# Optimization experiments

Hardware: AMD Instinct MI355X
Metric: run time of the kernel (lower is better)

The kernel has to match this reference:

```python
import jax, jax.numpy as jnp
import numpy as np

B, S, D, H, SPAN = 4, 1024, 768, 12, 512
HD = D // H  # 64


def setup_inputs() -> dict:
    key = jax.random.key(0)
    ks = jax.random.split(key, 8)
    hidden_states = jax.random.normal(ks[0], (B, S, D), jnp.float32)
    rel_embeddings = jax.random.normal(ks[1], (2 * SPAN, D), jnp.float32) * 0.02
    Wq = jax.random.normal(ks[2], (D, D), jnp.float32) * 0.02
    Wk = jax.random.normal(ks[3], (D, D), jnp.float32) * 0.02
    Wv = jax.random.normal(ks[4], (D, D), jnp.float32) * 0.02
    Wo = jax.random.normal(ks[5], (D, D), jnp.float32) * 0.02
    bq = jnp.zeros((D,), jnp.float32); bk = jnp.zeros((D,), jnp.float32)
    bv = jnp.zeros((D,), jnp.float32); bo = jnp.zeros((D,), jnp.float32)
    ln_g = jnp.ones((D,), jnp.float32); ln_b = jnp.zeros((D,), jnp.float32)
    idx = jnp.arange(S)
    relative_pos = (idx[:, None] - idx[None, :]).astype(jnp.int32)  # q - k
    lengths = jnp.array([1024, 896, 768, 512])  # padding-style mask
    valid = idx[None, :] < lengths[:, None]  # [B,S]
    attention_mask = (valid[:, :, None] & valid[:, None, :])[:, None, :, :].astype(jnp.int32)  # [B,1,S,S]
    return dict(hidden_states=hidden_states, rel_embeddings=rel_embeddings,
                Wq=Wq, bq=bq, Wk=Wk, bk=bk, Wv=Wv, bv=bv, Wo=Wo, bo=bo,
                ln_g=ln_g, ln_b=ln_b, attention_mask=attention_mask,
                relative_pos=relative_pos)


def reference(hidden_states, rel_embeddings, Wq, bq, Wk, bk, Wv, bv, Wo, bo,
              ln_g, ln_b, attention_mask, relative_pos):
    # content projections -> [B,H,S,HD]
    q = (hidden_states @ Wq.T + bq).reshape(B, S, H, HD).transpose(0, 2, 1, 3)
    k = (hidden_states @ Wk.T + bk).reshape(B, S, H, HD).transpose(0, 2, 1, 3)
    v = (hidden_states @ Wv.T + bv).reshape(B, S, H, HD).transpose(0, 2, 1, 3)

    scale_qk = jnp.sqrt(jnp.float32(HD * 3))  # scale_factor = 3
    scores = jnp.einsum('bhqd,bhkd->bhqk', q, k) / scale_qk

    # shared-key position projections -> [H, 2*SPAN, HD]
    pos_q = (rel_embeddings @ Wq.T + bq).reshape(2 * SPAN, H, HD).transpose(1, 0, 2)
    pos_k = (rel_embeddings @ Wk.T + bk).reshape(2 * SPAN, H, HD).transpose(1, 0, 2)

    rp = relative_pos.astype(jnp.int32)
    # c2p: query vs relative key-position embedding, gathered by clamp(rel+span)
    c2p_att = jnp.einsum('bhqd,hkd->bhqk', q, pos_k)  # [B,H,S,2*SPAN]
    c2p_pos = jnp.clip(rp + SPAN, 0, 2 * SPAN - 1)
    c2p_idx = jnp.broadcast_to(c2p_pos[None, None], (B, H, S, S))
    c2p = jnp.take_along_axis(c2p_att, c2p_idx, axis=-1) / scale_qk

    # p2c: key vs relative query-position embedding, gathered by clamp(-rel+span), then transposed
    p2c_att = jnp.einsum('bhkd,hqd->bhkq', k, pos_q)  # [B,H,S,2*SPAN]
    p2c_pos = jnp.clip(SPAN - rp, 0, 2 * SPAN - 1)
    p2c_idx = jnp.broadcast_to(p2c_pos[None, None], (B, H, S, S))
    p2c = jnp.swapaxes(jnp.take_along_axis(p2c_att, p2c_idx, axis=-1), -1, -2)
    p2c = p2c / jnp.sqrt(jnp.float32(HD))  # note: torch uses sqrt(d) here, no scale_factor

    scores = scores + c2p + p2c

    # XSoftmax: masked softmax with zeros at masked positions
    mask = attention_mask.astype(bool)  # [B,1,S,S]
    neg = jnp.finfo(scores.dtype).min
    probs = jax.nn.softmax(jnp.where(mask, scores, neg), axis=-1)
    probs = jnp.where(mask, probs, jnp.float32(0))

    ctx = jnp.einsum('bhqk,bhkd->bhqd', probs, v).transpose(0, 2, 1, 3).reshape(B, S, D)

    # DebertaV2SelfOutput: dense + residual + LayerNorm(eps=1e-7)
    x = ctx @ Wo.T + bo + hidden_states
    mu = x.mean(-1, keepdims=True)
    var = ((x - mu) ** 2).mean(-1, keepdims=True)
    return (x - mu) / jnp.sqrt(var + 1e-7) * ln_g + ln_b
```

## Files before the change

### kernel.cpp

```cpp
#include <hip/hip_runtime.h>
#include <hip/hip_bf16.h>
#include <stdint.h>

typedef __hip_bfloat16 bf16;
typedef __attribute__((ext_vector_type(8))) short s8v;
typedef __attribute__((ext_vector_type(4))) float f4v;

__device__ __align__(16) bf16 g_hidden[4096 * 768];
__device__ __align__(16) bf16 g_rel[1024 * 768];
__device__ __align__(16) bf16 g_Wqkv[2304 * 768];
__device__ __align__(16) bf16 g_Wo[768 * 768];
__device__ __align__(16) bf16 g_biasQKV[2304];
__device__ __align__(16) bf16 g_biasPos[1536];
__device__ __align__(16) bf16 g_bo[768];
__device__ __align__(16) bf16 g_lng[768];
__device__ __align__(16) bf16 g_lnb[768];
__device__ __align__(16) bf16 g_Y1[4096 * 1536];
__device__ __align__(16) bf16 g_VT[48u * 64 * 1024];
__device__ __align__(16) bf16 g_Yp[1024 * 1536];
__device__ __align__(16) bf16 g_ctx[4096 * 768];
__device__ __align__(16) float g_X[4096 * 768];
__device__ int g_vq[4096], g_vk[4096], g_kmax[4];

__device__ __forceinline__ float bfs(short x) {
  return __uint_as_float(((unsigned int)(unsigned short)x) << 16);
}
__device__ __forceinline__ unsigned short f2bf(float f) {
  bf16 h = __float2bfloat16(f);
  return *(unsigned short*)&h;
}
__device__ __forceinline__ bool detect_bf16(const void* lng_raw) {
  return *(const unsigned int*)lng_raw == 0x3F803F80u;
}

__device__ __forceinline__ void cvt4(const void* src, bf16* dst, long grp, bool isbf) {
  long e = grp * 4;
  if (isbf) {
    *(uint2*)(dst + e) = *(const uint2*)((const bf16*)src + e);
  } else {
    float4 f = *(const float4*)((const float*)src + e);
    union { unsigned short us[4]; uint2 v; } u;
    u.us[0] = f2bf(f.x); u.us[1] = f2bf(f.y); u.us[2] = f2bf(f.z); u.us[3] = f2bf(f.w);
    *(uint2*)(dst + e) = u.v;
  }
}

__global__ __launch_bounds__(256) void cvt_inputs(
    const void* h, const void* r,
    const void* wq, const void* wk, const void* wv, const void* wo,
    const void* bq, const void* bk, const void* bv, const void* bo,
    const void* lg, const void* lb)
{
  if (blockIdx.x == 0 && threadIdx.x < 4) g_kmax[threadIdx.x] = 0;
  const bool isbf = detect_bf16(lg);
  long i = (long)blockIdx.x * 256 + threadIdx.x;
  if (i < 786432) { cvt4(h,  g_hidden,          i, isbf); return; } i -= 786432;
  if (i < 196608) { cvt4(r,  g_rel,             i, isbf); return; } i -= 196608;
  if (i < 147456) { cvt4(wq, g_Wqkv,            i, isbf); return; } i -= 147456;
  if (i < 147456) { cvt4(wk, g_Wqkv + 589824,   i, isbf); return; } i -= 147456;
  if (i < 147456) { cvt4(wv, g_Wqkv + 1179648,  i, isbf); return; } i -= 147456;
  if (i < 147456) { cvt4(wo, g_Wo,              i, isbf); return; } i -= 147456;
  if (i < 192)    { cvt4(bq, g_biasQKV,         i, isbf); return; } i -= 192;
  if (i < 192)    { cvt4(bk, g_biasQKV + 768,   i, isbf); return; } i -= 192;
  if (i < 192)    { cvt4(bv, g_biasQKV + 1536,  i, isbf); return; } i -= 192;
  if (i < 192)    { cvt4(bq, g_biasPos,         i, isbf); return; } i -= 192;
  if (i < 192)    { cvt4(bk, g_biasPos + 768,   i, isbf); return; } i -= 192;
  if (i < 192)    { cvt4(lg, g_lng,             i, isbf); return; } i -= 192;
  if (i < 192)    { cvt4(lb, g_lnb,             i, isbf); return; }
}

__global__ __launch_bounds__(256) void mask_prep(const int* __restrict__ mask) {
  int t = blockIdx.x * 256 + threadIdx.x;
  int b = t >> 10, i = t & 1023;
  int vq = mask[((size_t)(b * 1024 + i)) * 1024];
  int vk = mask[((size_t)(b * 1024)) * 1024 + i];
  g_vq[t] = vq;
  g_vk[t] = vk;
  if (vq | vk) atomicMax(&g_kmax[b], i + 1);
}

__global__ __launch_bounds__(256, 2) void gemm_bt(int which) {
  __shared__ short As[128][72];
  __shared__ short Bs[128][72];

  const bf16 *A, *B; const bf16* bias;
  int lda, ldb, K, mode;
  const int m0 = blockIdx.y * 128, n0 = blockIdx.x * 128;

  if (which == 0) {
    A = g_hidden; lda = 768; B = g_Wqkv; ldb = 768; bias = g_biasQKV; K = 768;
    mode = (n0 >= 1536) ? 5 : 0;
  } else if (which == 1) {
    A = g_rel; lda = 768; B = g_Wqkv; ldb = 768; bias = g_biasPos; K = 768; mode = 1;
  } else {
    A = g_ctx; lda = 768; B = g_Wo; ldb = 768; bias = g_bo; K = 768; mode = 4;
  }

  const int tid = threadIdx.x, wave = tid >> 6, lane = tid & 63;
  const int quad = lane >> 4, l15 = lane & 15;
  const int wm = (wave >> 1) * 64, wn = (wave & 1) * 64;
  const int sr = tid >> 2, sc8 = (tid & 3) * 16;

  f4v acc[4][4];
#pragma unroll
  for (int i = 0; i < 4; i++)
#pragma unroll
    for (int j = 0; j < 4; j++) acc[i][j] = (f4v){0.f, 0.f, 0.f, 0.f};

  uint4 pa0, pa1, pa2, pa3, pb0, pb1, pb2, pb3;
#define LOAD_T(k0)                                                           \
  {                                                                          \
    const bf16* ap = A + (size_t)(m0 + sr) * lda + (k0) + sc8;               \
    const bf16* ap2 = A + (size_t)(m0 + sr + 64) * lda + (k0) + sc8;         \
    const bf16* bp = B + (size_t)(n0 + sr) * ldb + (k0) + sc8;               \
    const bf16* bp2 = B + (size_t)(n0 + sr + 64) * ldb + (k0) + sc8;         \
    pa0 = *(const uint4*)ap;  pa1 = *(const uint4*)(ap + 8);                 \
    pa2 = *(const uint4*)ap2; pa3 = *(const uint4*)(ap2 + 8);                \
    pb0 = *(const uint4*)bp;  pb1 = *(const uint4*)(bp + 8);                 \
    pb2 = *(const uint4*)bp2; pb3 = *(const uint4*)(bp2 + 8);                \
  }

  LOAD_T(0)
  for (int k0 = 0; k0 < K; k0 += 64) {
    __syncthreads();
    *(uint4*)&As[sr][sc8] = pa0;      *(uint4*)&As[sr][sc8 + 8] = pa1;
    *(uint4*)&As[sr + 64][sc8] = pa2; *(uint4*)&As[sr + 64][sc8 + 8] = pa3;
    *(uint4*)&Bs[sr][sc8] = pb0;      *(uint4*)&Bs[sr][sc8 + 8] = pb1;
    *(uint4*)&Bs[sr + 64][sc8] = pb2; *(uint4*)&Bs[sr + 64][sc8 + 8] = pb3;
    if (k0 + 64 < K) LOAD_T(k0 + 64)
    __syncthreads();

    s8v af[4][2], bfr[4][2];
#pragma unroll
    for (int mt = 0; mt < 4; mt++) {
      af[mt][0] = *(const s8v*)&As[wm + mt * 16 + l15][quad * 8];
      af[mt][1] = *(const s8v*)&As[wm + mt * 16 + l15][32 + quad * 8];
    }
#pragma unroll
    for (int nt = 0; nt < 4; nt++) {
      bfr[nt][0] = *(const s8v*)&Bs[wn + nt * 16 + l15][quad * 8];
      bfr[nt][1] = *(const s8v*)&Bs[wn + nt * 16 + l15][32 + quad * 8];
    }
#pragma unroll
    for (int mt = 0; mt < 4; mt++)
#pragma unroll
      for (int nt = 0; nt < 4; nt++) {
        acc[mt][nt] = __builtin_amdgcn_mfma_f32_16x16x32_bf16(af[mt][0], bfr[nt][0], acc[mt][nt], 0, 0, 0);
        acc[mt][nt] = __builtin_amdgcn_mfma_f32_16x16x32_bf16(af[mt][1], bfr[nt][1], acc[mt][nt], 0, 0, 0);
      }
  }
#undef LOAD_T

  float biasv[4];
#pragma unroll
  for (int nt = 0; nt < 4; nt++)
    biasv[nt] = bfs(*(const short*)&bias[n0 + wn + nt * 16 + l15]);

#pragma unroll
  for (int mt = 0; mt < 4; mt++) {
#pragma unroll
    for (int nt = 0; nt < 4; nt++) {
      const int mbase = m0 + wm + mt * 16 + quad * 4;
      const int n = n0 + wn + nt * 16 + l15;
      if (mode == 5) {
        const int dd = n - 1536, hv = dd >> 6, hd = dd & 63;
        const int bb = mbase >> 10, ss = mbase & 1023;
        float t0 = acc[mt][nt][0] + biasv[nt], t1 = acc[mt][nt][1] + biasv[nt];
        float t2 = acc[mt][nt][2] + biasv[nt], t3 = acc[mt][nt][3] + biasv[nt];
        uint2 pk;
        pk.x = (unsigned int)f2bf(t0) | ((unsigned int)f2bf(t1) << 16);
        pk.y = (unsigned int)f2bf(t2) | ((unsigned int)f2bf(t3) << 16);
        *(uint2*)(g_VT + (((size_t)(bb * 12 + hv) * 64 + hd) << 10) + ss) = pk;
        continue;
      }
#pragma unroll
      for (int reg = 0; reg < 4; reg++) {
        const int m = mbase + reg;
        float v = acc[mt][nt][reg] + biasv[nt];
        if (mode == 0) {
          g_Y1[(size_t)m * 1536 + n] = __float2bfloat16(v);
        } else if (mode == 1) {
          g_Yp[(size_t)m * 1536 + n] = __float2bfloat16(v);
        } else {
          v += bfs(*(const short*)&g_hidden[(size_t)m * 768 + n]);
          g_X[(size_t)m * 768 + n] = v;
        }
      }
    }
  }
}

__global__ __launch_bounds__(256, 2) void attn_mfma() {
  const int bh = blockIdx.y, b = bh / 12, hh = bh - b * 12;
  const int q0 = blockIdx.x * 64;
  const int tid = threadIdx.x, wave = tid >> 6, lane = tid & 63;
  const int quad = lane >> 4, l15 = lane & 15;
  const int kmax = g_kmax[b];

  if (q0 >= kmax) {
    uint4 zz = {0u, 0u, 0u, 0u};
#pragma unroll
    for (int s = tid; s < 512; s += 256) {
      int r = s >> 3, cc = (s & 7) * 8;
      *(uint4*)(g_ctx + (size_t)(b * 1024 + q0 + r) * 768 + hh * 64 + cc) = zz;
    }
    return;
  }

  __shared__ short Ks[64][72], VTs[64][72];
  __shared__ short BandA[128][72];
  __shared__ short BandB[128][72];
  __shared__ short Pl[4][16][72];
  short* C2Pl = &BandA[0][0];
  short* P2Cl = &BandB[0][0];

  const size_t qrow = (size_t)(b * 1024 + q0 + wave * 16 + l15) * 1536 + hh * 64;
  const s8v qf0 = *(const s8v*)(g_Y1 + qrow + quad * 8);
  const s8v qf1 = *(const s8v*)(g_Y1 + qrow + 32 + quad * 8);

  int vqr[4];
#pragma unroll
  for (int reg = 0; reg < 4; reg++)
    vqr[reg] = g_vq[b * 1024 + q0 + wave * 16 + quad * 4 + reg];

  f4v accO[4];
#pragma unroll
  for (int dt = 0; dt < 4; dt++) accO[dt] = (f4v){0.f, 0.f, 0.f, 0.f};
  float psum[4] = {0.f, 0.f, 0.f, 0.f};

  const int sr = tid >> 2, sc8 = (tid & 3) * 16;
  const int brow = tid >> 1, bcol = (tid & 1) * 32;
  const bf16* Kbase = g_Y1 + (size_t)(b * 1024) * 1536 + 768 + hh * 64;
  const bf16* Vbase = g_VT + ((size_t)bh << 16);
  const bf16* PKbase = g_Yp + 768 + hh * 64;
  const bf16* PQbase = g_Yp + hh * 64;

  uint4 rk0, rk1, rv0, rv1, rpk[4], rpq[4];
#define LOAD_A(k0)                                                         \
  {                                                                        \
    const bf16* kp = Kbase + (size_t)((k0) + sr) * 1536 + sc8;             \
    rk0 = *(const uint4*)kp; rk1 = *(const uint4*)(kp + 8);                \
    const bf16* vp = Vbase + ((size_t)sr << 10) + (k0) + sc8;              \
    rv0 = *(const uint4*)vp; rv1 = *(const uint4*)(vp + 8);                \
    int jk = min(max(q0 - (k0) + 449 + brow, 0), 1023);                    \
    const bf16* pk = PKbase + (size_t)jk * 1536 + bcol;                    \
    rpk[0] = *(const uint4*)pk;       rpk[1] = *(const uint4*)(pk + 8);    \
    rpk[2] = *(const uint4*)(pk + 16); rpk[3] = *(const uint4*)(pk + 24);  \
    int jq = min(max((k0) - q0 + 449 + brow, 0), 1023);                    \
    const bf16* pq = PQbase + (size_t)jq * 1536 + bcol;                    \
    rpq[0] = *(const uint4*)pq;       rpq[1] = *(const uint4*)(pq + 8);    \
    rpq[2] = *(const uint4*)(pq + 16); rpq[3] = *(const uint4*)(pq + 24);  \
  }

  LOAD_A(0)
  const float r192 = 0.0721687836487032f;
  const float r64 = 0.125f;

  for (int k0 = 0; k0 < kmax; k0 += 64) {
    __syncthreads();
    *(uint4*)&Ks[sr][sc8] = rk0;   *(uint4*)&Ks[sr][sc8 + 8] = rk1;
    *(uint4*)&VTs[sr][sc8] = rv0;  *(uint4*)&VTs[sr][sc8 + 8] = rv1;
    *(uint4*)&BandA[brow][bcol] = rpk[0];      *(uint4*)&BandA[brow][bcol + 8] = rpk[1];
    *(uint4*)&BandA[brow][bcol + 16] = rpk[2]; *(uint4*)&BandA[brow][bcol + 24] = rpk[3];
    *(uint4*)&BandB[brow][bcol] = rpq[0];      *(uint4*)&BandB[brow][bcol + 8] = rpq[1];
    *(uint4*)&BandB[brow][bcol + 16] = rpq[2]; *(uint4*)&BandB[brow][bcol + 24] = rpq[3];
    if (k0 + 64 < kmax) LOAD_A(k0 + 64)
    __syncthreads();

    const s8v ka0 = *(const s8v*)&Ks[wave * 16 + l15][quad * 8];
    const s8v ka1 = *(const s8v*)&Ks[wave * 16 + l15][32 + quad * 8];

    f4v cacc[8], pacc[8];
#pragma unroll
    for (int nt2 = 0; nt2 < 8; nt2++) {
      s8v b0 = *(const s8v*)&BandA[nt2 * 16 + l15][quad * 8];
      s8v b1 = *(const s8v*)&BandA[nt2 * 16 + l15][32 + quad * 8];
      cacc[nt2] = __builtin_amdgcn_mfma_f32_16x16x32_bf16(qf0, b0, (f4v){0.f, 0.f, 0.f, 0.f}, 0, 0, 0);
      cacc[nt2] = __builtin_amdgcn_mfma_f32_16x16x32_bf16(qf1, b1, cacc[nt2], 0, 0, 0);
      s8v c0 = *(const s8v*)&BandB[nt2 * 16 + l15][quad * 8];
      s8v c1 = *(const s8v*)&BandB[nt2 * 16 + l15][32 + quad * 8];
      pacc[nt2] = __builtin_amdgcn_mfma_f32_16x16x32_bf16(ka0, c0, (f4v){0.f, 0.f, 0.f, 0.f}, 0, 0, 0);
      pacc[nt2] = __builtin_amdgcn_mfma_f32_16x16x32_bf16(ka1, c1, pacc[nt2], 0, 0, 0);
    }

    f4v sacc[4];
#pragma unroll
    for (int nt = 0; nt < 4; nt++) {
      s8v kb0 = *(const s8v*)&Ks[nt * 16 + l15][quad * 8];
      s8v kb1 = *(const s8v*)&Ks[nt * 16 + l15][32 + quad * 8];
      sacc[nt] = __builtin_amdgcn_mfma_f32_16x16x32_bf16(qf0, kb0, (f4v){0.f, 0.f, 0.f, 0.f}, 0, 0, 0);
      sacc[nt] = __builtin_amdgcn_mfma_f32_16x16x32_bf16(qf1, kb1, sacc[nt], 0, 0, 0);
    }

    __syncthreads();
#pragma unroll
    for (int nt2 = 0; nt2 < 8; nt2++) {
      const int col = nt2 * 16 + l15;
#pragma unroll
      for (int reg = 0; reg < 4; reg++) {
        const int row = wave * 16 + quad * 4 + reg;
        C2Pl[row * 130 + col] = (short)f2bf(cacc[nt2][reg]);
        P2Cl[row * 130 + col] = (short)f2bf(pacc[nt2][reg]);
      }
    }
    __syncthreads();

    const bool tail = (k0 + 64 > kmax);
#pragma unroll
    for (int nt = 0; nt < 4; nt++) {
      const int kl = nt * 16 + l15;
#pragma unroll
      for (int reg = 0; reg < 4; reg++) {
        const int ql = wave * 16 + quad * 4 + reg;
        float c2 = bfs(C2Pl[ql * 130 + (ql - kl + 63)]);
        float p2 = bfs(P2Cl[kl * 130 + (kl - ql + 63)]);
        float sc = (sacc[nt][reg] + c2) * r192 + p2 * r64;
        float pe = __expf(fminf(sc, 60.f));
        if (tail && (k0 + kl >= kmax)) pe = 0.f;
        psum[reg] += pe;
        Pl[wave][quad * 4 + reg][kl] = (short)f2bf(pe);
      }
    }

    s8v pa0 = *(const s8v*)&Pl[wave][l15][quad * 8];
    s8v pa1 = *(const s8v*)&Pl[wave][l15][32 + quad * 8];
#pragma unroll
    for (int dt = 0; dt < 4; dt++) {
      s8v vb0 = *(const s8v*)&VTs[dt * 16 + l15][quad * 8];
      s8v vb1 = *(const s8v*)&VTs[dt * 16 + l15][32 + quad * 8];
      accO[dt] = __builtin_amdgcn_mfma_f32_16x16x32_bf16(pa0, vb0, accO[dt], 0, 0, 0);
      accO[dt] = __builtin_amdgcn_mfma_f32_16x16x32_bf16(pa1, vb1, accO[dt], 0, 0, 0);
    }
  }
#undef LOAD_A

#pragma unroll
  for (int off = 1; off < 16; off <<= 1)
#pragma unroll
    for (int reg = 0; reg < 4; reg++) psum[reg] += __shfl_xor(psum[reg], off);

  float inv[4];
#pragma unroll
  for (int reg = 0; reg < 4; reg++)
    inv[reg] = (vqr[reg] != 0 && psum[reg] > 0.f) ? 1.f / psum[reg] : 0.f;

#pragma unroll
  for (int dt = 0; dt < 4; dt++)
#pragma unroll
    for (int reg = 0; reg < 4; reg++) {
      float v = accO[dt][reg] * inv[reg];
      g_ctx[(size_t)(b * 1024 + q0 + wave * 16 + quad * 4 + reg) * 768 + hh * 64 + dt * 16 + l15] =
          __float2bfloat16(v);
    }
}

__global__ __launch_bounds__(256) void ln_kernel(const void* lng_raw, void* out) {
  const bool isbf = detect_bf16(lng_raw);
  const int row = blockIdx.x;
  const int tid = threadIdx.x;
  const float* xr = g_X + (size_t)row * 768;
  float x0 = xr[tid], x1 = xr[tid + 256], x2 = xr[tid + 512];
  float s = x0 + x1 + x2;
  float s2 = x0 * x0 + x1 * x1 + x2 * x2;
#pragma unroll
  for (int off = 32; off; off >>= 1) { s += __shfl_xor(s, off); s2 += __shfl_xor(s2, off); }
  __shared__ float red[2][4];
  int w = tid >> 6, ln = tid & 63;
  if (ln == 0) { red[0][w] = s; red[1][w] = s2; }
  __syncthreads();
  float ts = red[0][0] + red[0][1] + red[0][2] + red[0][3];
  float ts2 = red[1][0] + red[1][1] + red[1][2] + red[1][3];
  float mu = ts * (1.f / 768.f);
  float var = fmaxf(ts2 * (1.f / 768.f) - mu * mu, 0.f);
  float rstd = rsqrtf(var + 1e-7f);
#pragma unroll
  for (int q = 0; q < 3; q++) {
    int cidx = tid + q * 256;
    float xv = (q == 0) ? x0 : (q == 1 ? x1 : x2);
    float gg = bfs(*(const short*)&g_lng[cidx]);
    float bb = bfs(*(const short*)&g_lnb[cidx]);
    float val = (xv - mu) * rstd * gg + bb;
    if (isbf) ((bf16*)out)[(size_t)row * 768 + cidx] = __float2bfloat16(val);
    else      ((float*)out)[(size_t)row * 768 + cidx] = val;
  }
}

extern "C" void kernel_launch(void* const* d_in, const int* in_sizes, int n_in,
                              void* d_out, int out_size, void* d_ws, size_t ws_size,
                              hipStream_t stream) {
  const int* amask = (const int*)d_in[12];
  (void)d_ws; (void)ws_size; (void)in_sizes; (void)n_in; (void)out_size;

  cvt_inputs<<<dim3(6150), 256, 0, stream>>>(
      d_in[0], d_in[1], d_in[2], d_in[4], d_in[6], d_in[8],
      d_in[3], d_in[5], d_in[7], d_in[9], d_in[10], d_in[11]);
  mask_prep<<<dim3(16), 256, 0, stream>>>(amask);
  gemm_bt<<<dim3(18, 32, 1), 256, 0, stream>>>(0);
  gemm_bt<<<dim3(12, 8, 1), 256, 0, stream>>>(1);
  attn_mfma<<<dim3(16, 48), 256, 0, stream>>>();
  gemm_bt<<<dim3(6, 32, 1), 256, 0, stream>>>(4);
  ln_kernel<<<dim3(4096), 256, 0, stream>>>(d_in[10], d_out);
}
```

Before: 395.2 us.

## Precompute c2p/p2c position scores in a separate band GEMM, gather in attention

Adds a band_gemm kernel that computes the full query×position and key×position score matrices for each (batch, head) into global bf16 buffers, skipping tiles outside the valid band. The attention kernel then gathers c2p and p2c values directly from these buffers. This replaces the in-loop band MFMAs, the LDS staging and the extra barriers, and also lowers LDS usage so the launch bound can allow more blocks per CU. The cost is a large intermediate (about 200 MB written and then read with scattered per-element gathers), which adds global memory traffic.

New measurement: 379.2 us. 4.0% less time.

```diff
diff --git a/kernel.cpp b/kernel.cpp
--- a/kernel.cpp
+++ b/kernel.cpp
@@ -18,6 +18,8 @@
 __device__ __align__(16) bf16 g_Y1[4096 * 1536];
 __device__ __align__(16) bf16 g_VT[48u * 64 * 1024];
 __device__ __align__(16) bf16 g_Yp[1024 * 1536];
+__device__ __align__(16) bf16 g_C2P[48u * 1024 * 1024];
+__device__ __align__(16) bf16 g_P2C[48u * 1024 * 1024];
 __device__ __align__(16) bf16 g_ctx[4096 * 768];
 __device__ __align__(16) float g_X[4096 * 768];
 __device__ int g_vq[4096], g_vk[4096], g_kmax[4];
@@ -190,7 +192,77 @@
   }
 }
 
-__global__ __launch_bounds__(256, 2) void attn_mfma() {
+__global__ __launch_bounds__(256, 2) void band_gemm() {
+  const int z = blockIdx.z;
+  const int which = z / 48, bh = z % 48;
+  const int b = bh / 12, hh = bh - b * 12;
+  const int m0 = blockIdx.y * 128, n0 = blockIdx.x * 128;
+  const int kmax = g_kmax[b];
+  if (m0 >= kmax) return;
+  const int lo = max(0, m0 + 513 - kmax);
+  const int hi = min(1023, m0 + 639);
+  if (n0 + 127 < lo || n0 > hi) return;
+
+  const bf16* A = g_Y1 + (size_t)(b * 1024) * 1536 + (which ? 768 : 0) + hh * 64;
+  const bf16* Bp = g_Yp + (which ? 0 : 768) + hh * 64;
+  bf16* Cp = (which ? g_P2C : g_C2P) + ((size_t)bh << 20);
+
+  __shared__ short As[128][68], Bs[128][68];
+  const int tid = threadIdx.x, wave = tid >> 6, lane = tid & 63;
+  const int quad = lane >> 4, l15 = lane & 15;
+  const int wm = (wave >> 1) * 64, wn = (wave & 1) * 64;
+  const int sr = tid >> 2, sc = (tid & 3) * 16;
+
+  {
+    const bf16* a0 = A + (size_t)(m0 + sr) * 1536 + sc;
+    const bf16* a1 = A + (size_t)(m0 + sr + 64) * 1536 + sc;
+    const bf16* b0 = Bp + (size_t)(n0 + sr) * 1536 + sc;
+    const bf16* b1 = Bp + (size_t)(n0 + sr + 64) * 1536 + sc;
+    *(uint4*)&As[sr][sc]          = *(const uint4*)a0;
+    *(uint4*)&As[sr][sc + 8]      = *(const uint4*)(a0 + 8);
+    *(uint4*)&As[sr + 64][sc]     = *(const uint4*)a1;
+    *(uint4*)&As[sr + 64][sc + 8] = *(const uint4*)(a1 + 8);
+    *(uint4*)&Bs[sr][sc]          = *(const uint4*)b0;
+    *(uint4*)&Bs[sr][sc + 8]      = *(const uint4*)(b0 + 8);
+    *(uint4*)&Bs[sr + 64][sc]     = *(const uint4*)b1;
+    *(uint4*)&Bs[sr + 64][sc + 8] = *(const uint4*)(b1 + 8);
+  }
+  __syncthreads();
+
+  s8v af[4][2], bfr[4][2];
+#pragma unroll
+  for (int mt = 0; mt < 4; mt++) {
+    af[mt][0] = *(const s8v*)&As[wm + mt * 16 + l15][quad * 8];
+    af[mt][1] = *(const s8v*)&As[wm + mt * 16 + l15][32 + quad * 8];
+  }
+#pragma unroll
+  for (int nt = 0; nt < 4; nt++) {
+    bfr[nt][0] = *(const s8v*)&Bs[wn + nt * 16 + l15][quad * 8];
+    bfr[nt][1] = *(const s8v*)&Bs[wn + nt * 16 + l15][32 + quad * 8];
+  }
+
+  f4v acc[4][4];
+#pragma unroll
+  for (int mt = 0; mt < 4; mt++)
+#pragma unroll
+    for (int nt = 0; nt < 4; nt++) {
+      acc[mt][nt] = __builtin_amdgcn_mfma_f32_16x16x32_bf16(af[mt][0], bfr[nt][0], (f4v){0.f, 0.f, 0.f, 0.f}, 0, 0, 0);
+      acc[mt][nt] = __builtin_amdgcn_mfma_f32_16x16x32_bf16(af[mt][1], bfr[nt][1], acc[mt][nt], 0, 0, 0);
+    }
+
+#pragma unroll
+  for (int mt = 0; mt < 4; mt++)
+#pragma unroll
+    for (int nt = 0; nt < 4; nt++) {
+      const int m = m0 + wm + mt * 16 + quad * 4;
+      const int n = n0 + wn + nt * 16 + l15;
+#pragma unroll
+      for (int reg = 0; reg < 4; reg++)
+        Cp[(size_t)(m + reg) * 1024 + n] = __float2bfloat16(acc[mt][nt][reg]);
+    }
+}
+
+__global__ __launch_bounds__(256, 4) void attn_mfma() {
   const int bh = blockIdx.y, b = bh / 12, hh = bh - b * 12;
   const int q0 = blockIdx.x * 64;
   const int tid = threadIdx.x, wave = tid >> 6, lane = tid & 63;
@@ -207,12 +279,7 @@
     return;
   }
 
-  __shared__ short Ks[64][72], VTs[64][72];
-  __shared__ short BandA[128][72];
-  __shared__ short BandB[128][72];
-  __shared__ short Pl[4][16][72];
-  short* C2Pl = &BandA[0][0];
-  short* P2Cl = &BandB[0][0];
+  __shared__ short Ks[64][68], VTs[64][68], Pl[4][16][68];
 
   const size_t qrow = (size_t)(b * 1024 + q0 + wave * 16 + l15) * 1536 + hh * 64;
   const s8v qf0 = *(const s8v*)(g_Y1 + qrow + quad * 8);
@@ -229,27 +296,19 @@
   float psum[4] = {0.f, 0.f, 0.f, 0.f};
 
   const int sr = tid >> 2, sc8 = (tid & 3) * 16;
-  const int brow = tid >> 1, bcol = (tid & 1) * 32;
   const bf16* Kbase = g_Y1 + (size_t)(b * 1024) * 1536 + 768 + hh * 64;
   const bf16* Vbase = g_VT + ((size_t)bh << 16);
-  const bf16* PKbase = g_Yp + 768 + hh * 64;
-  const bf16* PQbase = g_Yp + hh * 64;
-
-  uint4 rk0, rk1, rv0, rv1, rpk[4], rpq[4];
+  const bf16* __restrict__ C2Pb = g_C2P + ((size_t)bh << 20);
+  const bf16* __restrict__ P2Cb = g_P2C + ((size_t)bh << 20);
+  const int qg = q0 + wave * 16 + quad * 4;
+
+  uint4 rk0, rk1, rv0, rv1;
 #define LOAD_A(k0)                                                         \
   {                                                                        \
     const bf16* kp = Kbase + (size_t)((k0) + sr) * 1536 + sc8;             \
     rk0 = *(const uint4*)kp; rk1 = *(const uint4*)(kp + 8);                \
     const bf16* vp = Vbase + ((size_t)sr << 10) + (k0) + sc8;              \
     rv0 = *(const uint4*)vp; rv1 = *(const uint4*)(vp + 8);                \
-    int jk = min(max(q0 - (k0) + 449 + brow, 0), 1023);                    \
-    const bf16* pk = PKbase + (size_t)jk * 1536 + bcol;                    \
-    rpk[0] = *(const uint4*)pk;       rpk[1] = *(const uint4*)(pk + 8);    \
-    rpk[2] = *(const uint4*)(pk + 16); rpk[3] = *(const uint4*)(pk + 24);  \
-    int jq = min(max((k0) - q0 + 449 + brow, 0), 1023);                    \
-    const bf16* pq = PQbase + (size_t)jq * 1536 + bcol;                    \
-    rpq[0] = *(const uint4*)pq;       rpq[1] = *(const uint4*)(pq + 8);    \
-    rpq[2] = *(const uint4*)(pq + 16); rpq[3] = *(const uint4*)(pq + 24);  \
   }
 
   LOAD_A(0)
@@ -260,28 +319,23 @@
     __syncthreads();
     *(uint4*)&Ks[sr][sc8] = rk0;   *(uint4*)&Ks[sr][sc8 + 8] = rk1;
     *(uint4*)&VTs[sr][sc8] = rv0;  *(uint4*)&VTs[sr][sc8 + 8] = rv1;
-    *(uint4*)&BandA[brow][bcol] = rpk[0];      *(uint4*)&BandA[brow][bcol + 8] = rpk[1];
-    *(uint4*)&BandA[brow][bcol + 16] = rpk[2]; *(uint4*)&BandA[brow][bcol + 24] = rpk[3];
-    *(uint4*)&BandB[brow][bcol] = rpq[0];      *(uint4*)&BandB[brow][bcol + 8] = rpq[1];
-    *(uint4*)&BandB[brow][bcol + 16] = rpq[2]; *(uint4*)&BandB[brow][bcol + 24] = rpq[3];
+
+    short c2s[16], p2s[16];
+#pragma unroll
+    for (int nt = 0; nt < 4; nt++) {
+      const int k = k0 + nt * 16 + l15;
+#pragma unroll
+      for (int reg = 0; reg < 4; reg++) {
+        const int d = qg + reg - k;
+        const int cc = min(max(d + 512, 0), 1023);
+        const int cp = min(max(512 - d, 0), 1023);
+        c2s[nt * 4 + reg] = *(const short*)(C2Pb + (((size_t)(qg + reg)) << 10) + cc);
+        p2s[nt * 4 + reg] = *(const short*)(P2Cb + (((size_t)k) << 10) + cp);
+      }
+    }
+
     if (k0 + 64 < kmax) LOAD_A(k0 + 64)
     __syncthreads();
-
-    const s8v ka0 = *(const s8v*)&Ks[wave * 16 + l15][quad * 8];
-    const s8v ka1 = *(const s8v*)&Ks[wave * 16 + l15][32 + quad * 8];
-
-    f4v cacc[8], pacc[8];
-#pragma unroll
-    for (int nt2 = 0; nt2 < 8; nt2++) {
-      s8v b0 = *(const s8v*)&BandA[nt2 * 16 + l15][quad * 8];
-      s8v b1 = *(const s8v*)&BandA[nt2 * 16 + l15][32 + quad * 8];
-      cacc[nt2] = __builtin_amdgcn_mfma_f32_16x16x32_bf16(qf0, b0, (f4v){0.f, 0.f, 0.f, 0.f}, 0, 0, 0);
-      cacc[nt2] = __builtin_amdgcn_mfma_f32_16x16x32_bf16(qf1, b1, cacc[nt2], 0, 0, 0);
-      s8v c0 = *(const s8v*)&BandB[nt2 * 16 + l15][quad * 8];
-      s8v c1 = *(const s8v*)&BandB[nt2 * 16 + l15][32 + quad * 8];
-      pacc[nt2] = __builtin_amdgcn_mfma_f32_16x16x32_bf16(ka0, c0, (f4v){0.f, 0.f, 0.f, 0.f}, 0, 0, 0);
-      pacc[nt2] = __builtin_amdgcn_mfma_f32_16x16x32_bf16(ka1, c1, pacc[nt2], 0, 0, 0);
-    }
 
     f4v sacc[4];
 #pragma unroll
@@ -292,28 +346,14 @@
       sacc[nt] = __builtin_amdgcn_mfma_f32_16x16x32_bf16(qf1, kb1, sacc[nt], 0, 0, 0);
     }
 
-    __syncthreads();
-#pragma unroll
-    for (int nt2 = 0; nt2 < 8; nt2++) {
-      const int col = nt2 * 16 + l15;
+    const bool tail = (k0 + 64 > kmax);
+#pragma unroll
+    for (int nt = 0; nt < 4; nt++) {
+      const int kl = nt * 16 + l15;
 #pragma unroll
       for (int reg = 0; reg < 4; reg++) {
-        const int row = wave * 16 + quad * 4 + reg;
-        C2Pl[row * 130 + col] = (short)f2bf(cacc[nt2][reg]);
-        P2Cl[row * 130 + col] = (short)f2bf(pacc[nt2][reg]);
-      }
-    }
-    __syncthreads();
-
-    const bool tail = (k0 + 64 > kmax);
-#pragma unroll
-    for (int nt = 0; nt < 4; nt++) {
-      const int kl = nt * 16 + l15;
-#pragma unroll
-      for (int reg = 0; reg < 4; reg++) {
-        const int ql = wave * 16 + quad * 4 + reg;
-        float c2 = bfs(C2Pl[ql * 130 + (ql - kl + 63)]);
-        float p2 = bfs(P2Cl[kl * 130 + (kl - ql + 63)]);
+        float c2 = bfs(c2s[nt * 4 + reg]);
+        float p2 = bfs(p2s[nt * 4 + reg]);
         float sc = (sacc[nt][reg] + c2) * r192 + p2 * r64;
         float pe = __expf(fminf(sc, 60.f));
         if (tail && (k0 + kl >= kmax)) pe = 0.f;
@@ -397,6 +437,7 @@
   mask_prep<<<dim3(16), 256, 0, stream>>>(amask);
   gemm_bt<<<dim3(18, 32, 1), 256, 0, stream>>>(0);
   gemm_bt<<<dim3(12, 8, 1), 256, 0, stream>>>(1);
+  band_gemm<<<dim3(8, 8, 96), 256, 0, stream>>>();
   attn_mfma<<<dim3(16, 48), 256, 0, stream>>>();
   gemm_bt<<<dim3(6, 32, 1), 256, 0, stream>>>(4);
   ln_kernel<<<dim3(4096), 256, 0, stream>>>(d_in[10], d_out);
```
